# Optimization experiments

Hardware: AMD Instinct MI355X
Metric: run time of the kernel (lower is better)

## Reference

```python
import jax, jax.numpy as jnp
import numpy as np

N_NODES = 100000
N_EDGES = 1600000
IN_CH = 64
HID = 64
OUT = 2


def sage_conv(x, src, dst, W_agg, W_root, b):
    # PyG SAGEConv (mean aggr): out = lin_l(mean_{j in N(i)} x_j) + lin_r(x_i)
    n = x.shape[0]
    msgs = x[src]                                        # [E, F] gather
    agg = jax.ops.segment_sum(msgs, dst, num_segments=n)  # [N, F] scatter-add
    cnt = jax.ops.segment_sum(jnp.ones((src.shape[0], 1), x.dtype), dst, num_segments=n)
    agg = agg / jnp.maximum(cnt, 1)                      # mean; isolated nodes -> 0
    return agg @ W_agg + x @ W_root + b


def setup_inputs() -> dict:
    key = jax.random.key(0)
    ks = jax.random.split(key, 8)
    s = lambda f: 1.0 / np.sqrt(f)
    x = jax.random.normal(ks[0], (N_NODES, IN_CH), dtype=jnp.float32)
    edge_index = jax.random.randint(ks[1], (2, N_EDGES), 0, N_NODES, dtype=jnp.int64)
    return {
        "x": x,
        "edge_index": edge_index,
        "W1_agg": jax.random.normal(ks[2], (IN_CH, HID), dtype=jnp.float32) * s(IN_CH),
        "W1_root": jax.random.normal(ks[3], (IN_CH, HID), dtype=jnp.float32) * s(IN_CH),
        "b1": jnp.zeros((HID,), jnp.float32),
        "W2_agg": jax.random.normal(ks[4], (HID, HID), dtype=jnp.float32) * s(HID),
        "W2_root": jax.random.normal(ks[5], (HID, HID), dtype=jnp.float32) * s(HID),
        "b2": jnp.zeros((HID,), jnp.float32),
        "W_lin": jax.random.normal(ks[6], (HID, OUT), dtype=jnp.float32) * s(HID),
        "b_lin": jnp.zeros((OUT,), jnp.float32),
    }


def reference(x, edge_index, W1_agg, W1_root, b1, W2_agg, W2_root, b2, W_lin, b_lin):
    src, dst = edge_index[0], edge_index[1]
    h = jax.nn.relu(sage_conv(x, src, dst, W1_agg, W1_root, b1))   # dropout = identity (eval)
    h = jax.nn.relu(sage_conv(h, src, dst, W2_agg, W2_root, b2))
    return h @ W_lin + b_lin
```

## Files before the change

kernel.cpp:

```cpp
#include <hip/hip_runtime.h>
#include <hip/hip_bf16.h>

#define FEAT 64
#define CHUNK 2048
#define MAX_NB 1024
#define SCAP 1792

typedef __attribute__((ext_vector_type(8))) short bf16x8;
typedef __attribute__((ext_vector_type(4))) float f32x4;
typedef __attribute__((ext_vector_type(2))) float f32x2;

__device__ __forceinline__ float bflo2f(unsigned int u) {
    union { unsigned int u; float f; } v; v.u = u << 16; return v.f;
}
__device__ __forceinline__ float bfhi2f(unsigned int u) {
    union { unsigned int u; float f; } v; v.u = u & 0xffff0000u; return v.f;
}
__device__ __forceinline__ unsigned short f2bf(float f) {
    union { float f; unsigned int u; } v; v.f = f;
    unsigned int u = v.u;
    u += 0x7fffu + ((u >> 16) & 1u);
    return (unsigned short)(u >> 16);
}
__device__ __forceinline__ f32x2 bfpair(unsigned int u) {
    f32x2 r; r.x = bflo2f(u & 0xffffu); r.y = bfhi2f(u); return r;
}

__global__ __launch_bounds__(256) void prep_kernel(
    const unsigned short* __restrict__ xh, const int* __restrict__ ei32,
    const void* __restrict__ w1a, const void* __restrict__ w1r,
    const void* __restrict__ b1,  const void* __restrict__ w2a,
    const void* __restrict__ w2r, const void* __restrict__ b2,
    const void* __restrict__ wl,  const void* __restrict__ bl,
    float* __restrict__ wbuf, unsigned short* __restrict__ Wt,
    int* __restrict__ flags, const void* __restrict__ x_in,
    unsigned short* __restrict__ x16, int n8) {
    __shared__ int cnt_bf, cnt_nz;
    int tid = threadIdx.x;
    if (tid == 0) { cnt_bf = 0; cnt_nz = 0; }
    __syncthreads();
    unsigned short h = xh[tid * 2];
    int e = (h >> 7) & 0xFF;
    if (e >= 110 && e <= 132) atomicAdd(&cnt_bf, 1);
    if (ei32[tid * 2 + 1] != 0) atomicAdd(&cnt_nz, 1);
    __syncthreads();
    int f0 = (cnt_bf >= 128) ? 1 : 0;
    if (blockIdx.x == 0 && tid == 0) {
        flags[0] = f0;
        flags[1] = (cnt_nz < 8) ? 1 : 0;
    }
    int i = blockIdx.x * 256 + tid;
    if (i < 16642) {
        const void* src; int off;
        if      (i < 4096)  { src = w1a; off = i; }
        else if (i < 8192)  { src = w1r; off = i - 4096; }
        else if (i < 8256)  { src = b1;  off = i - 8192; }
        else if (i < 12352) { src = w2a; off = i - 8256; }
        else if (i < 16448) { src = w2r; off = i - 12352; }
        else if (i < 16512) { src = b2;  off = i - 16448; }
        else if (i < 16640) { src = wl;  off = i - 16512; }
        else                { src = bl;  off = i - 16640; }
        float v = f0 ? bflo2f(((const unsigned short*)src)[off])
                     : ((const float*)src)[off];
        wbuf[i] = v;
        unsigned short hv = f2bf(v);
        if (i < 4096)                      Wt[(off & 63) * 128 + (off >> 6)] = hv;
        else if (i < 8192)                 Wt[(off & 63) * 128 + 64 + (off >> 6)] = hv;
        else if (i >= 8256 && i < 12352)   Wt[8192 + (off & 63) * 128 + (off >> 6)] = hv;
        else if (i >= 12352 && i < 16448)  Wt[8192 + (off & 63) * 128 + 64 + (off >> 6)] = hv;
    }
    if (!f0 && i < n8) {
        float4 a = ((const float4*)x_in)[2 * i];
        float4 b = ((const float4*)x_in)[2 * i + 1];
        uint4 o;
        o.x = (unsigned int)f2bf(a.x) | ((unsigned int)f2bf(a.y) << 16);
        o.y = (unsigned int)f2bf(a.z) | ((unsigned int)f2bf(a.w) << 16);
        o.z = (unsigned int)f2bf(b.x) | ((unsigned int)f2bf(b.y) << 16);
        o.w = (unsigned int)f2bf(b.z) | ((unsigned int)f2bf(b.w) << 16);
        ((uint4*)x16)[i] = o;
    }
}

__global__ __launch_bounds__(256) void p1_hist_kernel(
    const int* __restrict__ ei32, int* __restrict__ hist,
    int E, int N, int NB, int EC, const int* __restrict__ flags) {
    __shared__ int lh[MAX_NB];
    int tid = threadIdx.x, c = blockIdx.x;
    for (int i = tid; i < NB; i += 256) lh[i] = 0;
    __syncthreads();
    int idx64 = flags[1];
    long base = (long)c * CHUNK;
#pragma unroll 4
    for (int j = 0; j < CHUNK / 256; ++j) {
        long e = base + j * 256 + tid;
        if (e < E) {
            int d = idx64 ? ei32[2 * ((long)E + e)] : ei32[(long)E + e];
            if ((unsigned)d < (unsigned)N)
                atomicAdd(&lh[d >> 8], 1);
        }
    }
    __syncthreads();
    for (int k = tid; k < NB; k += 256) hist[(long)k * EC + c] = lh[k];
}

__global__ __launch_bounds__(256) void scan1_kernel(const int* __restrict__ in,
                                                    int* __restrict__ out,
                                                    int* __restrict__ blocksum, int n) {
    int tid = threadIdx.x;
    int base = blockIdx.x * 2048 + tid * 8;
    int v[8];
    int tsum = 0;
#pragma unroll
    for (int i = 0; i < 8; ++i) {
        v[i] = (base + i < n) ? in[base + i] : 0;
        tsum += v[i];
    }
    int lane = tid & 63;
    int x = tsum;
#pragma unroll
    for (int off = 1; off < 64; off <<= 1) {
        int y = __shfl_up(x, off);
        if (lane >= off) x += y;
    }
    __shared__ int wsum[4];
    int wave = tid >> 6;
    if (lane == 63) wsum[wave] = x;
    __syncthreads();
    int woff = 0;
#pragma unroll
    for (int w = 0; w < 4; ++w) if (w < wave) woff += wsum[w];
    int run = woff + x - tsum;
#pragma unroll
    for (int i = 0; i < 8; ++i) {
        if (base + i < n) out[base + i] = run;
        run += v[i];
    }
    if (tid == 255) blocksum[blockIdx.x] = woff + x;
}

__global__ __launch_bounds__(256) void scan3_kernel(int* __restrict__ out,
                                                    const int* __restrict__ blocksum, int n) {
    int bb = blockIdx.x, tid = threadIdx.x;
    __shared__ int wsum[4];
    __shared__ int spre;
    int s = 0;
    for (int b = tid; b < bb; b += 256) s += blocksum[b];
#pragma unroll
    for (int off = 32; off > 0; off >>= 1) s += __shfl_down(s, off);
    int lane = tid & 63, wave = tid >> 6;
    if (lane == 0) wsum[wave] = s;
    __syncthreads();
    if (tid == 0) spre = wsum[0] + wsum[1] + wsum[2] + wsum[3];
    __syncthreads();
    int pre = spre;
    int base = bb * 2048;
#pragma unroll
    for (int k = 0; k < 8; ++k) {
        int i = base + k * 256 + tid;
        if (i < n) out[i] += pre;
    }
}

__global__ __launch_bounds__(256) void p3_scatter_kernel(
    const int* __restrict__ ei32, const int* __restrict__ hscan,
    int* __restrict__ bkt, int E, int N, int NB, int EC,
    const int* __restrict__ flags) {
    __shared__ int lh[MAX_NB];
    int tid = threadIdx.x, c = blockIdx.x;
    for (int i = tid; i < NB; i += 256) lh[i] = 0;
    __syncthreads();
    int idx64 = flags[1];
    long base = (long)c * CHUNK;
#pragma unroll 4
    for (int j = 0; j < CHUNK / 256; ++j) {
        long e = base + j * 256 + tid;
        if (e < E) {
            int s = idx64 ? ei32[2 * e]             : ei32[e];
            int d = idx64 ? ei32[2 * ((long)E + e)] : ei32[(long)E + e];
            if ((unsigned)d < (unsigned)N) {
                if ((unsigned)s >= (unsigned)N) s = 0;
                int k = d >> 8;
                int r = atomicAdd(&lh[k], 1);
                bkt[hscan[(long)k * EC + c] + r] = s | ((d & 255) << 20);
            }
        }
    }
}

__global__ __launch_bounds__(256) void p4_build_kernel(
    const int* __restrict__ bkt, const int* __restrict__ hscan, const int* __restrict__ hist,
    int* __restrict__ offs, int* __restrict__ cnt, int* __restrict__ srcs,
    int E, int N, int NB, int EC) {
    int k = blockIdx.x, tid = threadIdx.x;
    int start = hscan[(long)k * EC];
    int end = (k + 1 < NB) ? hscan[(long)(k + 1) * EC]
                           : (hscan[(long)NB * EC - 1] + hist[(long)NB * EC - 1]);
    __shared__ int lc[256], lheads[256], wsum[4];
    lc[tid] = 0;
    __syncthreads();
    for (int e = start + tid; e < end; e += 256)
        atomicAdd(&lc[(bkt[e] >> 20) & 255], 1);
    __syncthreads();
    int cv = lc[tid];
    int lane = tid & 63, wave = tid >> 6;
    int x = cv;
#pragma unroll
    for (int off = 1; off < 64; off <<= 1) {
        int y = __shfl_up(x, off);
        if (lane >= off) x += y;
    }
    if (lane == 63) wsum[wave] = x;
    __syncthreads();
    int woff = 0;
#pragma unroll
    for (int w = 0; w < 4; ++w) if (w < wave) woff += wsum[w];
    int excl = woff + x - cv;
    int gnode = k * 256 + tid;
    if (gnode < N) { offs[gnode] = start + excl; cnt[gnode] = cv; }
    lheads[tid] = excl;
    __syncthreads();
    for (int e = start + tid; e < end; e += 256) {
        int p = bkt[e];
        int d8 = (p >> 20) & 255;
        int pos = start + atomicAdd(&lheads[d8], 1);
        srcs[pos] = p & 0xFFFFF;
    }
}

__global__ __launch_bounds__(256, 6) void sage_fused_kernel(
    const void* __restrict__ feat_raw, const unsigned short* __restrict__ feat_ws,
    const int* __restrict__ srcs, const int* __restrict__ offs,
    const int* __restrict__ cnt,
    const unsigned short* __restrict__ Wt, const float* __restrict__ bias,
    unsigned short* __restrict__ out16, int N,
    const float* __restrict__ wl, const float* __restrict__ bl,
    void* __restrict__ out_final, const int* __restrict__ flags, int sel) {

    const unsigned short* feat16 =
        (sel && !flags[0]) ? feat_ws : (const unsigned short*)feat_raw;

    __shared__ unsigned short A_l[64][136];
    __shared__ int srcs_l[SCAP];

    int tid = threadIdx.x;
    int blk = blockIdx.x;

    int first = blk * 64;
    int lastN = first + 63; if (lastN >= N) lastN = N - 1;
    int eb = offs[first];
    int eEnd = offs[lastN] + cnt[lastN];
    int nE = eEnd - eb; if (nE > SCAP) nE = SCAP;
    for (int i = tid; i < nE; i += 256) srcs_l[i] = srcs[eb + i];

#pragma unroll
    for (int i = 0; i < 2; ++i) {
        int ch = tid + i * 256;
        int r = ch >> 3, c = ch & 7;
        int row = blk * 64 + r;
        uint4 u = make_uint4(0, 0, 0, 0);
        if (row < N) u = ((const uint4*)(feat16 + (size_t)row * FEAT))[c];
        *(uint4*)&A_l[r][64 + c * 8] = u;
    }
    __syncthreads();

    int lane = tid & 63;
    int wave = tid >> 6;
    int g = lane >> 3;
    int li = lane & 7;

    for (int pass = 0; pass < 2; ++pass) {
        int r = pass * 32 + wave * 8 + g;
        int node = blk * 64 + r;
        f32x2 a0 = {0.f, 0.f}, a1 = a0, a2 = a0, a3 = a0;
        int deg = 0;
        if (node < N) {
            int start = offs[node];
            deg = cnt[node];
            int base = start - eb;
            if (base + deg <= SCAP) {
                int j = 0;
                for (; j + 4 <= deg; j += 4) {
                    int s0 = srcs_l[base + j];
                    int s1 = srcs_l[base + j + 1];
                    int s2 = srcs_l[base + j + 2];
                    int s3 = srcs_l[base + j + 3];
                    uint4 u0 = *(const uint4*)(feat16 + (size_t)s0 * FEAT + 8 * li);
                    uint4 u1 = *(const uint4*)(feat16 + (size_t)s1 * FEAT + 8 * li);
                    uint4 u2 = *(const uint4*)(feat16 + (size_t)s2 * FEAT + 8 * li);
                    uint4 u3 = *(const uint4*)(feat16 + (size_t)s3 * FEAT + 8 * li);
                    a0 += bfpair(u0.x); a1 += bfpair(u0.y); a2 += bfpair(u0.z); a3 += bfpair(u0.w);
                    a0 += bfpair(u1.x); a1 += bfpair(u1.y); a2 += bfpair(u1.z); a3 += bfpair(u1.w);
                    a0 += bfpair(u2.x); a1 += bfpair(u2.y); a2 += bfpair(u2.z); a3 += bfpair(u2.w);
                    a0 += bfpair(u3.x); a1 += bfpair(u3.y); a2 += bfpair(u3.z); a3 += bfpair(u3.w);
                }
                for (; j < deg; ++j) {
                    int s = srcs_l[base + j];
                    uint4 u = *(const uint4*)(feat16 + (size_t)s * FEAT + 8 * li);
                    a0 += bfpair(u.x); a1 += bfpair(u.y); a2 += bfpair(u.z); a3 += bfpair(u.w);
                }
            } else {
                int j = 0;
                for (; j + 4 <= deg; j += 4) {
                    int s0 = srcs[start + j];
                    int s1 = srcs[start + j + 1];
                    int s2 = srcs[start + j + 2];
                    int s3 = srcs[start + j + 3];
                    uint4 u0 = *(const uint4*)(feat16 + (size_t)s0 * FEAT + 8 * li);
                    uint4 u1 = *(const uint4*)(feat16 + (size_t)s1 * FEAT + 8 * li);
                    uint4 u2 = *(const uint4*)(feat16 + (size_t)s2 * FEAT + 8 * li);
                    uint4 u3 = *(const uint4*)(feat16 + (size_t)s3 * FEAT + 8 * li);
                    a0 += bfpair(u0.x); a1 += bfpair(u0.y); a2 += bfpair(u0.z); a3 += bfpair(u0.w);
                    a0 += bfpair(u1.x); a1 += bfpair(u1.y); a2 += bfpair(u1.z); a3 += bfpair(u1.w);
                    a0 += bfpair(u2.x); a1 += bfpair(u2.y); a2 += bfpair(u2.z); a3 += bfpair(u2.w);
                    a0 += bfpair(u3.x); a1 += bfpair(u3.y); a2 += bfpair(u3.z); a3 += bfpair(u3.w);
                }
                for (; j < deg; ++j) {
                    int s = srcs[start + j];
                    uint4 u = *(const uint4*)(feat16 + (size_t)s * FEAT + 8 * li);
                    a0 += bfpair(u.x); a1 += bfpair(u.y); a2 += bfpair(u.z); a3 += bfpair(u.w);
                }
            }
        }
        float inv = 1.0f / (float)(deg > 0 ? deg : 1);
        uint4 o;
        o.x = (unsigned)f2bf(a0.x * inv) | ((unsigned)f2bf(a0.y * inv) << 16);
        o.y = (unsigned)f2bf(a1.x * inv) | ((unsigned)f2bf(a1.y * inv) << 16);
        o.z = (unsigned)f2bf(a2.x * inv) | ((unsigned)f2bf(a2.y * inv) << 16);
        o.w = (unsigned)f2bf(a3.x * inv) | ((unsigned)f2bf(a3.y * inv) << 16);
        *(uint4*)&A_l[r][8 * li] = o;
    }
    __syncthreads();

    int r0 = wave * 16;
    int m = lane & 15, quad = lane >> 4;

    f32x4 acc0 = {0.f, 0.f, 0.f, 0.f};
    f32x4 acc1 = acc0, acc2 = acc0, acc3 = acc0;

#pragma unroll
    for (int k0 = 0; k0 < 128; k0 += 32) {
        bf16x8 a  = *(const bf16x8*)&A_l[r0 + m][k0 + quad * 8];
        bf16x8 b0 = *(const bf16x8*)(Wt + ( 0 + m) * 128 + k0 + quad * 8);
        bf16x8 b1 = *(const bf16x8*)(Wt + (16 + m) * 128 + k0 + quad * 8);
        bf16x8 b2 = *(const bf16x8*)(Wt + (32 + m) * 128 + k0 + quad * 8);
        bf16x8 b3 = *(const bf16x8*)(Wt + (48 + m) * 128 + k0 + quad * 8);
        acc0 = __builtin_amdgcn_mfma_f32_16x16x32_bf16(a, b0, acc0, 0, 0, 0);
        acc1 = __builtin_amdgcn_mfma_f32_16x16x32_bf16(a, b1, acc1, 0, 0, 0);
        acc2 = __builtin_amdgcn_mfma_f32_16x16x32_bf16(a, b2, acc2, 0, 0, 0);
        acc3 = __builtin_amdgcn_mfma_f32_16x16x32_bf16(a, b3, acc3, 0, 0, 0);
    }
    __syncthreads();

#pragma unroll
    for (int c = 0; c < 4; ++c) {
        f32x4 av = (c == 0) ? acc0 : (c == 1) ? acc1 : (c == 2) ? acc2 : acc3;
        float bv = bias[c * 16 + m];
#pragma unroll
        for (int reg = 0; reg < 4; ++reg) {
            float v = fmaxf(av[reg] + bv, 0.f);
            A_l[r0 + quad * 4 + reg][c * 16 + m] = f2bf(v);
        }
    }
    __syncthreads();

    if (out16) {
#pragma unroll
        for (int i = 0; i < 2; ++i) {
            int ch = tid + i * 256;
            int r = ch >> 3, c = ch & 7;
            int row = blk * 64 + r;
            if (row < N)
                ((uint4*)(out16 + (size_t)row * FEAT))[c] = *(const uint4*)&A_l[r][c * 8];
        }
    }

    if (wl) {
        int r = tid >> 2, part = tid & 3;
        int row = blk * 64 + r;
        if (row < N) {
            float p0 = 0.f, p1 = 0.f;
#pragma unroll
            for (int j = 0; j < 16; ++j) {
                int f = part * 16 + j;
                float v = bflo2f(A_l[r][f]);
                p0 += v * wl[f * 2 + 0];
                p1 += v * wl[f * 2 + 1];
            }
            p0 += __shfl_down(p0, 2, 4); p0 += __shfl_down(p0, 1, 4);
            p1 += __shfl_down(p1, 2, 4); p1 += __shfl_down(p1, 1, 4);
            if (part == 0) {
                p0 += bl[0];
                p1 += bl[1];
                if (flags[0]) {
                    unsigned int o = ((unsigned int)f2bf(p1) << 16) | (unsigned int)f2bf(p0);
                    ((unsigned int*)out_final)[row] = o;
                } else {
                    ((float2*)out_final)[row] = make_float2(p0, p1);
                }
            }
        }
    }
}

extern "C" void kernel_launch(void* const* d_in, const int* in_sizes, int n_in,
                              void* d_out, int out_size, void* d_ws, size_t ws_size,
                              hipStream_t stream) {
    const void* x_in = d_in[0];
    const int*  ei32 = (const int*)d_in[1];

    int N = in_sizes[0] / FEAT;
    int E = in_sizes[1] / 2;
    int NB = (N + 255) >> 8;
    int EC = (E + CHUNK - 1) / CHUNK;
    int HN = NB * EC;

    unsigned short* x16   = (unsigned short*)d_ws;
    unsigned short* h16   = x16 + (size_t)N * FEAT;
    unsigned short* Wt    = h16 + (size_t)N * FEAT;
    float*          wbuf  = (float*)(Wt + 16384);
    int*            hist  = (int*)(wbuf + 16704);
    int*            hscan = hist + HN;
    int*            bsum  = hscan + HN;
    int*            flags = bsum + 1024;
    int*            offs  = flags + 16;
    int*            cnt   = offs + N;
    int*            bkt   = cnt + N;
    int*            srcs  = bkt + E;

    float* b1_32 = wbuf + 8192;
    float* b2_32 = wbuf + 16448;
    float* wl32  = wbuf + 16512;
    float* bl32  = wbuf + 16640;

    int n8 = N * FEAT / 8;
    int pBlocks = (n8 + 255) / 256;
    if (pBlocks < 66) pBlocks = 66;
    prep_kernel<<<pBlocks, 256, 0, stream>>>(
        (const unsigned short*)x_in, ei32,
        d_in[2], d_in[3], d_in[4], d_in[5], d_in[6], d_in[7], d_in[8], d_in[9],
        wbuf, Wt, flags, x_in, x16, n8);

    p1_hist_kernel<<<EC, 256, 0, stream>>>(ei32, hist, E, N, NB, EC, flags);
    int sB = (HN + 2047) / 2048;
    scan1_kernel<<<sB, 256, 0, stream>>>(hist, hscan, bsum, HN);
    scan3_kernel<<<sB, 256, 0, stream>>>(hscan, bsum, HN);
    p3_scatter_kernel<<<EC, 256, 0, stream>>>(ei32, hscan, bkt, E, N, NB, EC, flags);
    p4_build_kernel<<<NB, 256, 0, stream>>>(bkt, hscan, hist, offs, cnt, srcs, E, N, NB, EC);

    int gBlocks = (N + 63) / 64;

    sage_fused_kernel<<<gBlocks, 256, 0, stream>>>(
        x_in, x16, srcs, offs, cnt, Wt, b1_32, h16, N,
        nullptr, nullptr, nullptr, flags, 1);

    sage_fused_kernel<<<gBlocks, 256, 0, stream>>>(
        h16, h16, srcs, offs, cnt, Wt + 8192, b2_32, nullptr, N,
        wl32, bl32, d_out, flags, 0);
}
```

Baseline: 240.7 us.

## Fuse histogram into prep kernel, interleave two-node gathers, enlarge edge chunks

Merges the per-chunk destination histogram into the prep launch as extra blocks, which recompute the index-width flag locally, so one kernel launch and one dependency go away. CHUNK grows from 2048 to 8192, cutting the number of histogram columns and the size of the scan. The aggregation loop now walks both of a thread's nodes together, so more independent feature loads are in flight at once. It also drops the occupancy hint from launch bounds, which may raise register use, and the larger chunks mean fewer blocks for the histogram and scatter passes.

```diff
diff --git a/kernel.cpp b/kernel.cpp
--- a/kernel.cpp
+++ b/kernel.cpp
@@ -2,7 +2,7 @@
 #include <hip/hip_bf16.h>
 
 #define FEAT 64
-#define CHUNK 2048
+#define CHUNK 8192
 #define MAX_NB 1024
 #define SCAP 1792
 
@@ -26,7 +26,7 @@
     f32x2 r; r.x = bflo2f(u & 0xffffu); r.y = bfhi2f(u); return r;
 }
 
-__global__ __launch_bounds__(256) void prep_kernel(
+__global__ __launch_bounds__(256) void prep_p1_kernel(
     const unsigned short* __restrict__ xh, const int* __restrict__ ei32,
     const void* __restrict__ w1a, const void* __restrict__ w1r,
     const void* __restrict__ b1,  const void* __restrict__ w2a,
@@ -34,9 +34,35 @@
     const void* __restrict__ wl,  const void* __restrict__ bl,
     float* __restrict__ wbuf, unsigned short* __restrict__ Wt,
     int* __restrict__ flags, const void* __restrict__ x_in,
-    unsigned short* __restrict__ x16, int n8) {
+    unsigned short* __restrict__ x16, int n8,
+    int* __restrict__ hist, int E, int N, int NB, int EC, int pB) {
+    __shared__ int lh[MAX_NB];
     __shared__ int cnt_bf, cnt_nz;
     int tid = threadIdx.x;
+
+    if (blockIdx.x >= pB) {
+        int c = blockIdx.x - pB;
+        if (tid == 0) cnt_nz = 0;
+        for (int i = tid; i < NB; i += 256) lh[i] = 0;
+        __syncthreads();
+        if (ei32[tid * 2 + 1] != 0) atomicAdd(&cnt_nz, 1);
+        __syncthreads();
+        int idx64 = (cnt_nz < 8) ? 1 : 0;
+        long base = (long)c * CHUNK;
+#pragma unroll 4
+        for (int j = 0; j < CHUNK / 256; ++j) {
+            long e = base + j * 256 + tid;
+            if (e < E) {
+                int d = idx64 ? ei32[2 * ((long)E + e)] : ei32[(long)E + e];
+                if ((unsigned)d < (unsigned)N)
+                    atomicAdd(&lh[d >> 8], 1);
+            }
+        }
+        __syncthreads();
+        for (int k = tid; k < NB; k += 256) hist[(long)k * EC + c] = lh[k];
+        return;
+    }
+
     if (tid == 0) { cnt_bf = 0; cnt_nz = 0; }
     __syncthreads();
     unsigned short h = xh[tid * 2];
@@ -81,28 +107,6 @@
     }
 }
 
-__global__ __launch_bounds__(256) void p1_hist_kernel(
-    const int* __restrict__ ei32, int* __restrict__ hist,
-    int E, int N, int NB, int EC, const int* __restrict__ flags) {
-    __shared__ int lh[MAX_NB];
-    int tid = threadIdx.x, c = blockIdx.x;
-    for (int i = tid; i < NB; i += 256) lh[i] = 0;
-    __syncthreads();
-    int idx64 = flags[1];
-    long base = (long)c * CHUNK;
-#pragma unroll 4
-    for (int j = 0; j < CHUNK / 256; ++j) {
-        long e = base + j * 256 + tid;
-        if (e < E) {
-            int d = idx64 ? ei32[2 * ((long)E + e)] : ei32[(long)E + e];
-            if ((unsigned)d < (unsigned)N)
-                atomicAdd(&lh[d >> 8], 1);
-        }
-    }
-    __syncthreads();
-    for (int k = tid; k < NB; k += 256) hist[(long)k * EC + c] = lh[k];
-}
-
 __global__ __launch_bounds__(256) void scan1_kernel(const int* __restrict__ in,
                                                     int* __restrict__ out,
                                                     int* __restrict__ blocksum, int n) {
@@ -227,7 +231,11 @@
     }
 }
 
-__global__ __launch_bounds__(256, 6) void sage_fused_kernel(
+#define ACC8(acc0, acc1, acc2, acc3, u) \
+    acc0 += bfpair((u).x); acc1 += bfpair((u).y); \
+    acc2 += bfpair((u).z); acc3 += bfpair((u).w);
+
+__global__ __launch_bounds__(256) void sage_fused_kernel(
     const void* __restrict__ feat_raw, const unsigned short* __restrict__ feat_ws,
     const int* __restrict__ srcs, const int* __restrict__ offs,
     const int* __restrict__ cnt,
@@ -268,66 +276,80 @@
     int g = lane >> 3;
     int li = lane & 7;
 
-    for (int pass = 0; pass < 2; ++pass) {
-        int r = pass * 32 + wave * 8 + g;
-        int node = blk * 64 + r;
+    {
+        int rA = wave * 8 + g, rB = rA + 32;
+        int nodeA = blk * 64 + rA, nodeB = blk * 64 + rB;
+        int degA = 0, degB = 0;
+        const int* pA = srcs;
+        const int* pB = srcs;
+        if (nodeA < N) {
+            int st = offs[nodeA]; degA = cnt[nodeA];
+            int ba = st - eb;
+            pA = (ba + degA <= nE) ? (const int*)(srcs_l + ba) : (srcs + st);
+        }
+        if (nodeB < N) {
+            int st = offs[nodeB]; degB = cnt[nodeB];
+            int bb = st - eb;
+            pB = (bb + degB <= nE) ? (const int*)(srcs_l + bb) : (srcs + st);
+        }
         f32x2 a0 = {0.f, 0.f}, a1 = a0, a2 = a0, a3 = a0;
-        int deg = 0;
-        if (node < N) {
-            int start = offs[node];
-            deg = cnt[node];
-            int base = start - eb;
-            if (base + deg <= SCAP) {
-                int j = 0;
-                for (; j + 4 <= deg; j += 4) {
-                    int s0 = srcs_l[base + j];
-                    int s1 = srcs_l[base + j + 1];
-                    int s2 = srcs_l[base + j + 2];
-                    int s3 = srcs_l[base + j + 3];
-                    uint4 u0 = *(const uint4*)(feat16 + (size_t)s0 * FEAT + 8 * li);
-                    uint4 u1 = *(const uint4*)(feat16 + (size_t)s1 * FEAT + 8 * li);
-                    uint4 u2 = *(const uint4*)(feat16 + (size_t)s2 * FEAT + 8 * li);
-                    uint4 u3 = *(const uint4*)(feat16 + (size_t)s3 * FEAT + 8 * li);
-                    a0 += bfpair(u0.x); a1 += bfpair(u0.y); a2 += bfpair(u0.z); a3 += bfpair(u0.w);
-                    a0 += bfpair(u1.x); a1 += bfpair(u1.y); a2 += bfpair(u1.z); a3 += bfpair(u1.w);
-                    a0 += bfpair(u2.x); a1 += bfpair(u2.y); a2 += bfpair(u2.z); a3 += bfpair(u2.w);
-                    a0 += bfpair(u3.x); a1 += bfpair(u3.y); a2 += bfpair(u3.z); a3 += bfpair(u3.w);
-                }
-                for (; j < deg; ++j) {
-                    int s = srcs_l[base + j];
-                    uint4 u = *(const uint4*)(feat16 + (size_t)s * FEAT + 8 * li);
-                    a0 += bfpair(u.x); a1 += bfpair(u.y); a2 += bfpair(u.z); a3 += bfpair(u.w);
-                }
-            } else {
-                int j = 0;
-                for (; j + 4 <= deg; j += 4) {
-                    int s0 = srcs[start + j];
-                    int s1 = srcs[start + j + 1];
-                    int s2 = srcs[start + j + 2];
-                    int s3 = srcs[start + j + 3];
-                    uint4 u0 = *(const uint4*)(feat16 + (size_t)s0 * FEAT + 8 * li);
-                    uint4 u1 = *(const uint4*)(feat16 + (size_t)s1 * FEAT + 8 * li);
-                    uint4 u2 = *(const uint4*)(feat16 + (size_t)s2 * FEAT + 8 * li);
-                    uint4 u3 = *(const uint4*)(feat16 + (size_t)s3 * FEAT + 8 * li);
-                    a0 += bfpair(u0.x); a1 += bfpair(u0.y); a2 += bfpair(u0.z); a3 += bfpair(u0.w);
-                    a0 += bfpair(u1.x); a1 += bfpair(u1.y); a2 += bfpair(u1.z); a3 += bfpair(u1.w);
-                    a0 += bfpair(u2.x); a1 += bfpair(u2.y); a2 += bfpair(u2.z); a3 += bfpair(u2.w);
-                    a0 += bfpair(u3.x); a1 += bfpair(u3.y); a2 += bfpair(u3.z); a3 += bfpair(u3.w);
-                }
-                for (; j < deg; ++j) {
-                    int s = srcs[start + j];
-                    uint4 u = *(const uint4*)(feat16 + (size_t)s * FEAT + 8 * li);
-                    a0 += bfpair(u.x); a1 += bfpair(u.y); a2 += bfpair(u.z); a3 += bfpair(u.w);
-                }
-            }
-        }
-        float inv = 1.0f / (float)(deg > 0 ? deg : 1);
-        uint4 o;
-        o.x = (unsigned)f2bf(a0.x * inv) | ((unsigned)f2bf(a0.y * inv) << 16);
-        o.y = (unsigned)f2bf(a1.x * inv) | ((unsigned)f2bf(a1.y * inv) << 16);
-        o.z = (unsigned)f2bf(a2.x * inv) | ((unsigned)f2bf(a2.y * inv) << 16);
-        o.w = (unsigned)f2bf(a3.x * inv) | ((unsigned)f2bf(a3.y * inv) << 16);
-        *(uint4*)&A_l[r][8 * li] = o;
+        f32x2 b0 = a0, b1 = a0, b2 = a0, b3 = a0;
+
+        int dmin = degA < degB ? degA : degB;
+        int j = 0;
+        for (; j + 2 <= dmin; j += 2) {
+            int sA0 = pA[j], sA1 = pA[j + 1];
+            int sB0 = pB[j], sB1 = pB[j + 1];
+            uint4 uA0 = *(const uint4*)(feat16 + (size_t)sA0 * FEAT + 8 * li);
+            uint4 uA1 = *(const uint4*)(feat16 + (size_t)sA1 * FEAT + 8 * li);
+            uint4 uB0 = *(const uint4*)(feat16 + (size_t)sB0 * FEAT + 8 * li);
+            uint4 uB1 = *(const uint4*)(feat16 + (size_t)sB1 * FEAT + 8 * li);
+            ACC8(a0, a1, a2, a3, uA0); ACC8(a0, a1, a2, a3, uA1);
+            ACC8(b0, b1, b2, b3, uB0); ACC8(b0, b1, b2, b3, uB1);
+        }
+        int jA = j, jB = j;
+        for (; jA + 4 <= degA; jA += 4) {
+            int s0 = pA[jA], s1 = pA[jA + 1], s2 = pA[jA + 2], s3 = pA[jA + 3];
+            uint4 u0 = *(const uint4*)(feat16 + (size_t)s0 * FEAT + 8 * li);
+            uint4 u1 = *(const uint4*)(feat16 + (size_t)s1 * FEAT + 8 * li);
+            uint4 u2 = *(const uint4*)(feat16 + (size_t)s2 * FEAT + 8 * li);
+            uint4 u3 = *(const uint4*)(feat16 + (size_t)s3 * FEAT + 8 * li);
+            ACC8(a0, a1, a2, a3, u0); ACC8(a0, a1, a2, a3, u1);
+            ACC8(a0, a1, a2, a3, u2); ACC8(a0, a1, a2, a3, u3);
+        }
+        for (; jA < degA; ++jA) {
+            int s = pA[jA];
+            uint4 u = *(const uint4*)(feat16 + (size_t)s * FEAT + 8 * li);
+            ACC8(a0, a1, a2, a3, u);
+        }
+        for (; jB + 4 <= degB; jB += 4) {
+            int s0 = pB[jB], s1 = pB[jB + 1], s2 = pB[jB + 2], s3 = pB[jB + 3];
+            uint4 u0 = *(const uint4*)(feat16 + (size_t)s0 * FEAT + 8 * li);
+            uint4 u1 = *(const uint4*)(feat16 + (size_t)s1 * FEAT + 8 * li);
+            uint4 u2 = *(const uint4*)(feat16 + (size_t)s2 * FEAT + 8 * li);
+            uint4 u3 = *(const uint4*)(feat16 + (size_t)s3 * FEAT + 8 * li);
+            ACC8(b0, b1, b2, b3, u0); ACC8(b0, b1, b2, b3, u1);
+            ACC8(b0, b1, b2, b3, u2); ACC8(b0, b1, b2, b3, u3);
+        }
+        for (; jB < degB; ++jB) {
+            int s = pB[jB];
+            uint4 u = *(const uint4*)(feat16 + (size_t)s * FEAT + 8 * li);
+            ACC8(b0, b1, b2, b3, u);
+        }
+
+        float invA = 1.0f / (float)(degA > 0 ? degA : 1);
+        float invB = 1.0f / (float)(degB > 0 ? degB : 1);
+        uint4 oA, oB;
+        oA.x = (unsigned)f2bf(a0.x * invA) | ((unsigned)f2bf(a0.y * invA) << 16);
+        oA.y = (unsigned)f2bf(a1.x * invA) | ((unsigned)f2bf(a1.y * invA) << 16);
+        oA.z = (unsigned)f2bf(a2.x * invA) | ((unsigned)f2bf(a2.y * invA) << 16);
+        oA.w = (unsigned)f2bf(a3.x * invA) | ((unsigned)f2bf(a3.y * invA) << 16);
+        oB.x = (unsigned)f2bf(b0.x * invB) | ((unsigned)f2bf(b0.y * invB) << 16);
+        oB.y = (unsigned)f2bf(b1.x * invB) | ((unsigned)f2bf(b1.y * invB) << 16);
+        oB.z = (unsigned)f2bf(b2.x * invB) | ((unsigned)f2bf(b2.y * invB) << 16);
+        oB.w = (unsigned)f2bf(b3.x * invB) | ((unsigned)f2bf(b3.y * invB) << 16);
+        *(uint4*)&A_l[rA][8 * li] = oA;
+        *(uint4*)&A_l[rB][8 * li] = oB;
     }
     __syncthreads();
 
@@ -340,14 +362,14 @@
 #pragma unroll
     for (int k0 = 0; k0 < 128; k0 += 32) {
         bf16x8 a  = *(const bf16x8*)&A_l[r0 + m][k0 + quad * 8];
-        bf16x8 b0 = *(const bf16x8*)(Wt + ( 0 + m) * 128 + k0 + quad * 8);
-        bf16x8 b1 = *(const bf16x8*)(Wt + (16 + m) * 128 + k0 + quad * 8);
-        bf16x8 b2 = *(const bf16x8*)(Wt + (32 + m) * 128 + k0 + quad * 8);
-        bf16x8 b3 = *(const bf16x8*)(Wt + (48 + m) * 128 + k0 + quad * 8);
-        acc0 = __builtin_amdgcn_mfma_f32_16x16x32_bf16(a, b0, acc0, 0, 0, 0);
-        acc1 = __builtin_amdgcn_mfma_f32_16x16x32_bf16(a, b1, acc1, 0, 0, 0);
-        acc2 = __builtin_amdgcn_mfma_f32_16x16x32_bf16(a, b2, acc2, 0, 0, 0);
-        acc3 = __builtin_amdgcn_mfma_f32_16x16x32_bf16(a, b3, acc3, 0, 0, 0);
+        bf16x8 w0 = *(const bf16x8*)(Wt + ( 0 + m) * 128 + k0 + quad * 8);
+        bf16x8 w1 = *(const bf16x8*)(Wt + (16 + m) * 128 + k0 + quad * 8);
+        bf16x8 w2 = *(const bf16x8*)(Wt + (32 + m) * 128 + k0 + quad * 8);
+        bf16x8 w3 = *(const bf16x8*)(Wt + (48 + m) * 128 + k0 + quad * 8);
+        acc0 = __builtin_amdgcn_mfma_f32_16x16x32_bf16(a, w0, acc0, 0, 0, 0);
+        acc1 = __builtin_amdgcn_mfma_f32_16x16x32_bf16(a, w1, acc1, 0, 0, 0);
+        acc2 = __builtin_amdgcn_mfma_f32_16x16x32_bf16(a, w2, acc2, 0, 0, 0);
+        acc3 = __builtin_amdgcn_mfma_f32_16x16x32_bf16(a, w3, acc3, 0, 0, 0);
     }
     __syncthreads();
 
@@ -435,12 +457,12 @@
     int n8 = N * FEAT / 8;
     int pBlocks = (n8 + 255) / 256;
     if (pBlocks < 66) pBlocks = 66;
-    prep_kernel<<<pBlocks, 256, 0, stream>>>(
+    prep_p1_kernel<<<pBlocks + EC, 256, 0, stream>>>(
         (const unsigned short*)x_in, ei32,
         d_in[2], d_in[3], d_in[4], d_in[5], d_in[6], d_in[7], d_in[8], d_in[9],
-        wbuf, Wt, flags, x_in, x16, n8);
-
-    p1_hist_kernel<<<EC, 256, 0, stream>>>(ei32, hist, E, N, NB, EC, flags);
+        wbuf, Wt, flags, x_in, x16, n8,
+        hist, E, N, NB, EC, pBlocks);
+
     int sB = (HN + 2047) / 2048;
     scan1_kernel<<<sB, 256, 0, stream>>>(hist, hscan, bsum, HN);
     scan3_kernel<<<sB, 256, 0, stream>>>(hscan, bsum, HN);
```

After: 249.8 us. 3.8% more time.
